# Kernel optimization log

Measured on AMD Instinct MI355X. Metric: run time of the kernel, lower is better.

The kernel has to match this reference:

```python
import math
import jax, jax.numpy as jnp
import numpy as np

N = 50000          # nodes
E = 1_600_000      # edges
DNE = 128
DED = 128
NUM_RBF = 50
R_CUT = 5.0
LN_EPS = 1e-5


def setup_inputs() -> dict:
    key = jax.random.key(0)
    ks = jax.random.split(key, 16)
    z = jax.random.normal(ks[0], (N, 25), jnp.float32)
    edge = jax.random.randint(ks[1], (E, 2), 0, N, dtype=jnp.int64)
    r = jax.random.uniform(ks[2], (E,), jnp.float32) * (R_CUT * 1.1)  # some beyond cutoff
    u_raw = jax.random.normal(ks[3], (E, 3), jnp.float32)
    u = u_raw / jnp.linalg.norm(u_raw, axis=-1, keepdims=True)

    def xavier(k, shape):
        fan_in, fan_out = shape
        lim = math.sqrt(6.0 / (fan_in + fan_out))
        return jax.random.uniform(k, shape, jnp.float32, -lim, lim)

    return {
        "z": z, "edge": edge, "r": r, "u": u,
        "A_na_w": xavier(ks[4], (25, DNE)), "A_na_b": jnp.zeros((DNE,), jnp.float32),
        "A_nbr_w": xavier(ks[5], (25, DNE)), "A_nbr_b": jnp.zeros((DNE,), jnp.float32),
        "W_ndp_w": xavier(ks[6], (NUM_RBF, DNE)), "W_ndp_b": jnp.zeros((DNE,), jnp.float32),
        "W_nrd_w": xavier(ks[7], (2 * DNE, DNE)), "W_nrd_b": jnp.zeros((DNE,), jnp.float32),
        "W_nru_w": xavier(ks[8], (DNE, DNE)), "W_nru_b": jnp.zeros((DNE,), jnp.float32),
        "W_erp_w": xavier(ks[9], (NUM_RBF, DED)), "W_erp_b": jnp.zeros((DED,), jnp.float32),
        "ln_g": jnp.ones((DNE,), jnp.float32), "ln_b": jnp.zeros((DNE,), jnp.float32),
    }


def _sh_l2(u):
    x, y, zc = u[:, 0], u[:, 1], u[:, 2]
    s3 = math.sqrt(3.0)
    return jnp.stack([
        s3 * x * y,
        s3 * y * zc,
        0.5 * (3.0 * zc * zc - 1.0),
        s3 * zc * x,
        0.5 * s3 * (x * x - y * y),
    ], axis=-1)  # [E, 5]


def _rbf(r):
    start = math.exp(-R_CUT)
    means = jnp.linspace(start, 1.0, NUM_RBF)
    beta = (2.0 / NUM_RBF * (1.0 - start)) ** (-2)
    alpha = 5.0 / R_CUT
    return jnp.exp(-beta * (jnp.exp(-alpha * r[:, None]) - means) ** 2)  # [E, NUM_RBF]


def reference(z, edge, r, u,
              A_na_w, A_na_b, A_nbr_w, A_nbr_b,
              W_ndp_w, W_ndp_b, W_nrd_w, W_nrd_b,
              W_nru_w, W_nru_b, W_erp_w, W_erp_b,
              ln_g, ln_b):
    i, j = edge[:, 0], edge[:, 1]
    n_nodes = z.shape[0]

    # edge tensor representations (Lmax=2)
    rt0 = r[:, None]          # [E,1]
    rt1 = u                   # [E,3]
    rt2 = _sh_l2(u)           # [E,5]

    rbf = _rbf(r)                                              # [E,R]
    c = (0.5 * (jnp.cos(math.pi * r / R_CUT) + 1.0)
         * (r < R_CUT).astype(r.dtype))[:, None]               # [E,1]

    nbr = jax.nn.silu(z @ A_nbr_w + A_nbr_b)                   # [N,dne]
    gate = (rbf @ W_ndp_w + W_ndp_b) * c                       # [E,dne]
    msg = nbr[j] * gate                                        # gather + gate
    m = jax.ops.segment_sum(msg, i, num_segments=n_nodes)      # scatter-add [N,dne]

    na = jax.nn.silu(z @ A_na_w + A_na_b)
    h = jnp.concatenate([na, m], axis=-1) @ W_nrd_w + W_nrd_b  # [N,dne]
    mu = jnp.mean(h, axis=-1, keepdims=True)
    var = jnp.var(h, axis=-1, keepdims=True)
    h = (h - mu) / jnp.sqrt(var + LN_EPS) * ln_g + ln_b
    h = jax.nn.silu(h)
    h = h @ W_nru_w + W_nru_b                                  # [N,dne]

    t = (h[i] + h[j]) * (rbf @ W_erp_w + W_erp_b)              # [E,ded]
    return (h, t, rt0, rt1, rt2, c)
```

## Files before the change

### kernel.cpp

```cpp
#include <hip/hip_runtime.h>
#include <hip/hip_bf16.h>
#include <math.h>

#define NN 50000
#define NE 1600000
#define D 128
#define NRBF 50
#define RCUT 5.0f
#define LNEPS 1e-5f
#define EB 16
#define EB2 64
#define EDGE_GRID 2048
#define SCAN_B 196
#define NB 16
#define NPB 8

typedef __attribute__((ext_vector_type(8))) short bf16x8;
typedef __attribute__((ext_vector_type(4))) float f32x4;

__device__ __forceinline__ float silu_f(float x) {
    return x / (1.0f + __expf(-x));
}
__device__ __forceinline__ unsigned short f2bf(float x) {
    __hip_bfloat16 b = __float2bfloat16(x);
    return *reinterpret_cast<unsigned short*>(&b);
}
__device__ __forceinline__ float bf2f(unsigned short u) {
    unsigned int x = ((unsigned int)u) << 16;
    return __uint_as_float(x);
}

__global__ __launch_bounds__(128) void nbr_kernel(
    const float* __restrict__ z, const float* __restrict__ Aw,
    const float* __restrict__ Ab, unsigned short* __restrict__ nbr_bf)
{
    const int n = blockIdx.x;
    const int d = threadIdx.x;
    float acc = Ab[d];
#pragma unroll
    for (int k = 0; k < 25; ++k)
        acc = fmaf(z[n * 25 + k], Aw[k * D + d], acc);
    nbr_bf[(size_t)n * D + d] = f2bf(silu_f(acc));
}

__global__ __launch_bounds__(256) void aux_kernel(
    const int* __restrict__ edge, const float* __restrict__ r,
    const float* __restrict__ u, float* __restrict__ rt0,
    float* __restrict__ rt1, float* __restrict__ rt2,
    float* __restrict__ cout, int* __restrict__ cnt)
{
    const int e = blockIdx.x * 256 + threadIdx.x;
    if (e >= NE) return;
    const float rr = r[e];
    rt0[e] = rr;
    const float cc = (rr < RCUT)
        ? 0.5f * (__cosf(3.14159265358979f * rr * (1.0f / RCUT)) + 1.0f)
        : 0.0f;
    cout[e] = cc;
    const float x  = u[e * 3 + 0];
    const float y  = u[e * 3 + 1];
    const float zc = u[e * 3 + 2];
    rt1[(size_t)e * 3 + 0] = x;
    rt1[(size_t)e * 3 + 1] = y;
    rt1[(size_t)e * 3 + 2] = zc;
    const float s3 = 1.7320508075688772f;
    rt2[(size_t)e * 5 + 0] = s3 * x * y;
    rt2[(size_t)e * 5 + 1] = s3 * y * zc;
    rt2[(size_t)e * 5 + 2] = 0.5f * (3.0f * zc * zc - 1.0f);
    rt2[(size_t)e * 5 + 3] = s3 * zc * x;
    rt2[(size_t)e * 5 + 4] = 0.5f * s3 * (x * x - y * y);
    atomicAdd(&cnt[edge[2 * e]], 1);
}

__global__ __launch_bounds__(256) void scan1_kernel(
    const int* __restrict__ cnt, int* __restrict__ off, int* __restrict__ bsum)
{
    __shared__ int s[2][256];
    const int t = threadIdx.x;
    const int g = blockIdx.x * 256 + t;
    const int v = (g < NN) ? cnt[g] : 0;
    int incl = v;
    s[0][t] = incl;
    __syncthreads();
    int cur = 0;
#pragma unroll
    for (int dd = 1; dd < 256; dd <<= 1) {
        const int add = (t >= dd) ? s[cur][t - dd] : 0;
        incl += add;
        s[cur ^ 1][t] = incl;
        __syncthreads();
        cur ^= 1;
    }
    if (g < NN) off[g] = incl - v;
    if (t == 255) bsum[blockIdx.x] = incl;
}

__global__ __launch_bounds__(256) void scan2_kernel(int* __restrict__ bsum)
{
    __shared__ int s[2][256];
    const int t = threadIdx.x;
    const int v = (t < SCAN_B) ? bsum[t] : 0;
    int incl = v;
    s[0][t] = incl;
    __syncthreads();
    int cur = 0;
#pragma unroll
    for (int dd = 1; dd < 256; dd <<= 1) {
        const int add = (t >= dd) ? s[cur][t - dd] : 0;
        incl += add;
        s[cur ^ 1][t] = incl;
        __syncthreads();
        cur ^= 1;
    }
    if (t < SCAN_B) bsum[t] = incl - v;
}

__global__ __launch_bounds__(256) void scan3_kernel(
    int* __restrict__ off, const int* __restrict__ bsum)
{
    const int g = blockIdx.x * 256 + threadIdx.x;
    if (g < NN) off[g] += bsum[blockIdx.x];
    if (g == 0) off[NN] = NE;
}

__global__ __launch_bounds__(256) void scatter_kernel(
    const int* __restrict__ edge, const float* __restrict__ r,
    const int* __restrict__ off, int* __restrict__ cursor,
    uint2* __restrict__ jr)
{
    const int e = blockIdx.x * 256 + threadIdx.x;
    if (e >= NE) return;
    const int2 ep = ((const int2*)edge)[e];
    const int pos = atomicAdd(&cursor[ep.x], 1);
    uint2 v;
    v.x = (unsigned int)ep.y;
    v.y = __float_as_uint(r[e]);
    jr[off[ep.x] + pos] = v;
}

__global__ __launch_bounds__(128) void gather_msg_mfma(
    const uint2* __restrict__ jr, const int* __restrict__ off,
    const float* __restrict__ W_ndp, const float* __restrict__ b_ndp,
    const unsigned short* __restrict__ nbr_bf, float* __restrict__ m)
{
    __shared__ unsigned short P[EB][64];
    __shared__ float er_s[EB];
    __shared__ float c_s[EB];
    __shared__ int   j_s[EB];

    const int tid = threadIdx.x;
    const int w   = tid >> 6;
    const int l   = tid & 63;
    const int lr  = l & 15;
    const int lg  = l >> 4;

    bf16x8 wf[4][2];
#pragma unroll
    for (int dt = 0; dt < 4; ++dt) {
        const int col = w * 64 + lr * 4 + dt;
#pragma unroll
        for (int s = 0; s < 2; ++s) {
            bf16x8 v;
#pragma unroll
            for (int j = 0; j < 8; ++j) {
                const int k = s * 32 + lg * 8 + j;
                float wv = 0.0f;
                if (k < NRBF)       wv = W_ndp[k * D + col];
                else if (k == NRBF) wv = b_ndp[col];
                v[j] = (short)f2bf(wv);
            }
            wf[dt][s] = v;
        }
    }

    const float start = expf(-RCUT);
    const float step  = (1.0f - start) / (NRBF - 1);
    const float bq    = (2.0f / NRBF) * (1.0f - start);
    const float beta  = 1.0f / (bq * bq);

    const int prow = tid >> 3;
    const int pci  = tid & 7;

    for (int nn = 0; nn < NPB; ++nn) {
        const int n   = blockIdx.x * NPB + nn;
        const int s0  = off[n];
        const int deg = off[n + 1] - s0;

        f32x4 macc[4] = {{0,0,0,0},{0,0,0,0},{0,0,0,0},{0,0,0,0}};

        for (int base = 0; base < deg; base += EB) {
            const int chunk = min(EB, deg - base);
            if (tid < EB) {
                if (tid < chunk) {
                    const uint2 v = jr[s0 + base + tid];
                    const float rr = __uint_as_float(v.y);
                    er_s[tid] = __expf(-rr);
                    c_s[tid] = (rr < RCUT)
                        ? 0.5f * (__cosf(3.14159265358979f * rr * (1.0f / RCUT)) + 1.0f)
                        : 0.0f;
                    j_s[tid] = (int)v.x;
                } else {
                    er_s[tid] = 0.0f; c_s[tid] = 0.0f; j_s[tid] = 0;
                }
            }
            __syncthreads();
            {
                const float er = er_s[prow];
                const float cc = c_s[prow];
                unsigned int pk[4];
#pragma unroll
                for (int p2 = 0; p2 < 4; ++p2) {
                    unsigned int word = 0;
#pragma unroll
                    for (int c = 0; c < 2; ++c) {
                        const int k = pci * 8 + p2 * 2 + c;
                        float v = 0.0f;
                        if (k < NRBF) {
                            const float diff = er - (start + (float)k * step);
                            v = cc * __expf(-beta * diff * diff);
                        } else if (k == NRBF) {
                            v = cc;
                        }
                        word |= ((unsigned int)f2bf(v)) << (16 * c);
                    }
                    pk[p2] = word;
                }
                const int swc = pci ^ (prow & 7);
                *(uint4*)&P[prow][swc * 8] = make_uint4(pk[0], pk[1], pk[2], pk[3]);
            }
            __syncthreads();
            bf16x8 af[2];
#pragma unroll
            for (int s = 0; s < 2; ++s) {
                const int swc = (s * 4 + lg) ^ (lr & 7);
                af[s] = *(const bf16x8*)&P[lr][swc * 8];
            }
            f32x4 accs[4];
#pragma unroll
            for (int dt = 0; dt < 4; ++dt) {
                f32x4 acc = {0.0f, 0.0f, 0.0f, 0.0f};
                acc = __builtin_amdgcn_mfma_f32_16x16x32_bf16(af[0], wf[dt][0], acc, 0, 0, 0);
                acc = __builtin_amdgcn_mfma_f32_16x16x32_bf16(af[1], wf[dt][1], acc, 0, 0, 0);
                accs[dt] = acc;
            }
#pragma unroll
            for (int q = 0; q < 4; ++q) {
                const int row = j_s[lg * 4 + q];
                const uint2 nv8 = *(const uint2*)(nbr_bf + (size_t)row * D + w * 64 + lr * 4);
                const float n0 = bf2f((unsigned short)(nv8.x & 0xffff));
                const float n1 = bf2f((unsigned short)(nv8.x >> 16));
                const float n2 = bf2f((unsigned short)(nv8.y & 0xffff));
                const float n3 = bf2f((unsigned short)(nv8.y >> 16));
                macc[0][q] = fmaf(n0, accs[0][q], macc[0][q]);
                macc[1][q] = fmaf(n1, accs[1][q], macc[1][q]);
                macc[2][q] = fmaf(n2, accs[2][q], macc[2][q]);
                macc[3][q] = fmaf(n3, accs[3][q], macc[3][q]);
            }
            __syncthreads();
        }

        float v0 = macc[0][0] + macc[0][1] + macc[0][2] + macc[0][3];
        float v1 = macc[1][0] + macc[1][1] + macc[1][2] + macc[1][3];
        float v2 = macc[2][0] + macc[2][1] + macc[2][2] + macc[2][3];
        float v3 = macc[3][0] + macc[3][1] + macc[3][2] + macc[3][3];
        v0 += __shfl_xor(v0, 16); v0 += __shfl_xor(v0, 32);
        v1 += __shfl_xor(v1, 16); v1 += __shfl_xor(v1, 32);
        v2 += __shfl_xor(v2, 16); v2 += __shfl_xor(v2, 32);
        v3 += __shfl_xor(v3, 16); v3 += __shfl_xor(v3, 32);
        if (lg == 0) {
            float4 o = {v0, v1, v2, v3};
            *(float4*)&m[(size_t)n * D + w * 64 + lr * 4] = o;
        }
    }
}

__global__ __launch_bounds__(256) void node_kernel2(
    const float* __restrict__ z, const float* __restrict__ A_na_w,
    const float* __restrict__ A_na_b, const float* __restrict__ m,
    const float* __restrict__ W_nrd_w, const float* __restrict__ W_nrd_b,
    const float* __restrict__ W_nru_w, const float* __restrict__ W_nru_b,
    const float* __restrict__ ln_g, const float* __restrict__ ln_b,
    float* __restrict__ hout, unsigned short* __restrict__ h_bf)
{
    __shared__ float inbuf[NB][260];
    __shared__ float wbuf[32][128];
    __shared__ float part[4][NB][2];

    const int tid = threadIdx.x;
    const int n0 = blockIdx.x * NB;
    const int nl = tid & 15;
    const int dg = tid >> 4;

    for (int idx = tid; idx < NB * 128; idx += 256) {
        const int n = idx >> 7;
        const int d = idx & 127;
        float acc = A_na_b[d];
#pragma unroll
        for (int k = 0; k < 25; ++k)
            acc = fmaf(z[(size_t)(n0 + n) * 25 + k], A_na_w[k * D + d], acc);
        inbuf[n][d]       = silu_f(acc);
        inbuf[n][128 + d] = m[(size_t)(n0 + n) * D + d];
    }

    float h1[8];
#pragma unroll
    for (int dd = 0; dd < 8; ++dd) h1[dd] = W_nrd_b[dg * 8 + dd];

    for (int tile = 0; tile < 8; ++tile) {
        __syncthreads();
        for (int v = tid; v < 32 * 32; v += 256) {
            const int row = v >> 5;
            const int c4  = (v & 31) * 4;
            *(float4*)&wbuf[row][c4] =
                *(const float4*)&W_nrd_w[(size_t)(tile * 32 + row) * D + c4];
        }
        __syncthreads();
#pragma unroll 4
        for (int k = 0; k < 32; ++k) {
            const float rin = inbuf[nl][tile * 32 + k];
            const float4 wa = *(const float4*)&wbuf[k][dg * 8];
            const float4 wb = *(const float4*)&wbuf[k][dg * 8 + 4];
            h1[0] = fmaf(rin, wa.x, h1[0]);
            h1[1] = fmaf(rin, wa.y, h1[1]);
            h1[2] = fmaf(rin, wa.z, h1[2]);
            h1[3] = fmaf(rin, wa.w, h1[3]);
            h1[4] = fmaf(rin, wb.x, h1[4]);
            h1[5] = fmaf(rin, wb.y, h1[5]);
            h1[6] = fmaf(rin, wb.z, h1[6]);
            h1[7] = fmaf(rin, wb.w, h1[7]);
        }
    }

    float s = 0.0f, sq = 0.0f;
#pragma unroll
    for (int dd = 0; dd < 8; ++dd) { s += h1[dd]; sq += h1[dd] * h1[dd]; }
    s  += __shfl_xor(s, 16);  sq += __shfl_xor(sq, 16);
    s  += __shfl_xor(s, 32);  sq += __shfl_xor(sq, 32);
    const int wv = tid >> 6;
    if ((tid & 63) < 16) { part[wv][nl][0] = s; part[wv][nl][1] = sq; }
    __syncthreads();
    float ts = 0.0f, tsq = 0.0f;
#pragma unroll
    for (int w = 0; w < 4; ++w) { ts += part[w][nl][0]; tsq += part[w][nl][1]; }
    const float mu  = ts * (1.0f / 128.0f);
    const float var = tsq * (1.0f / 128.0f) - mu * mu;
    const float inv = rsqrtf(var + LNEPS);

#pragma unroll
    for (int dd = 0; dd < 8; ++dd) {
        const int d = dg * 8 + dd;
        inbuf[nl][d] = silu_f((h1[dd] - mu) * inv * ln_g[d] + ln_b[d]);
    }

    float h2[8];
#pragma unroll
    for (int dd = 0; dd < 8; ++dd) h2[dd] = W_nru_b[dg * 8 + dd];

    for (int tile = 0; tile < 4; ++tile) {
        __syncthreads();
        for (int v = tid; v < 32 * 32; v += 256) {
            const int row = v >> 5;
            const int c4  = (v & 31) * 4;
            *(float4*)&wbuf[row][c4] =
                *(const float4*)&W_nru_w[(size_t)(tile * 32 + row) * D + c4];
        }
        __syncthreads();
#pragma unroll 4
        for (int k = 0; k < 32; ++k) {
            const float rin = inbuf[nl][tile * 32 + k];
            const float4 wa = *(const float4*)&wbuf[k][dg * 8];
            const float4 wb = *(const float4*)&wbuf[k][dg * 8 + 4];
            h2[0] = fmaf(rin, wa.x, h2[0]);
            h2[1] = fmaf(rin, wa.y, h2[1]);
            h2[2] = fmaf(rin, wa.z, h2[2]);
            h2[3] = fmaf(rin, wa.w, h2[3]);
            h2[4] = fmaf(rin, wb.x, h2[4]);
            h2[5] = fmaf(rin, wb.y, h2[5]);
            h2[6] = fmaf(rin, wb.z, h2[6]);
            h2[7] = fmaf(rin, wb.w, h2[7]);
        }
    }

    float4 o0 = {h2[0], h2[1], h2[2], h2[3]};
    float4 o1 = {h2[4], h2[5], h2[6], h2[7]};
    *(float4*)&hout[(size_t)(n0 + nl) * D + dg * 8]     = o0;
    *(float4*)&hout[(size_t)(n0 + nl) * D + dg * 8 + 4] = o1;

    unsigned int b0 = (unsigned int)f2bf(h2[0]) | ((unsigned int)f2bf(h2[1]) << 16);
    unsigned int b1 = (unsigned int)f2bf(h2[2]) | ((unsigned int)f2bf(h2[3]) << 16);
    unsigned int b2 = (unsigned int)f2bf(h2[4]) | ((unsigned int)f2bf(h2[5]) << 16);
    unsigned int b3 = (unsigned int)f2bf(h2[6]) | ((unsigned int)f2bf(h2[7]) << 16);
    *(uint4*)&h_bf[(size_t)(n0 + nl) * D + dg * 8] = make_uint4(b0, b1, b2, b3);
}

__global__ __launch_bounds__(256) void edge_out_mfma(
    const int* __restrict__ edge, const float* __restrict__ r,
    const float* __restrict__ W_erp, const float* __restrict__ b_erp,
    const unsigned short* __restrict__ h_bf, float* __restrict__ t)
{
    __shared__ unsigned short P[EB2][64];
    __shared__ unsigned short hv[EB2][136];
    __shared__ int ij_s[EB2][2];

    const int tid = threadIdx.x;
    const int w  = tid >> 6;
    const int l  = tid & 63;
    const int lr = l & 15;
    const int lg = l >> 4;

    bf16x8 wf[8][2];
    float bias[8];
#pragma unroll
    for (int dt = 0; dt < 8; ++dt) {
        const int col = lr * 8 + dt;
        bias[dt] = b_erp[col];
#pragma unroll
        for (int s = 0; s < 2; ++s) {
            bf16x8 v;
#pragma unroll
            for (int j = 0; j < 8; ++j) {
                const int k = s * 32 + lg * 8 + j;
                v[j] = (k < NRBF) ? (short)f2bf(W_erp[k * D + col]) : (short)0;
            }
            wf[dt][s] = v;
        }
    }

    const float start = expf(-RCUT);
    const float step  = (1.0f - start) / (NRBF - 1);
    const float bq    = (2.0f / NRBF) * (1.0f - start);
    const float beta  = 1.0f / (bq * bq);

    const int prow  = tid & 63;
    const int kbase = (tid >> 6) * 16;

    const int nbatch = NE / EB2;
    for (int batch = blockIdx.x; batch < nbatch; batch += gridDim.x) {
        const int eb = batch * EB2;
        if (tid < EB2) {
            const int2 ep = ((const int2*)edge)[eb + tid];
            ij_s[tid][0] = ep.x;
            ij_s[tid][1] = ep.y;
        }
        {
            const float er = __expf(-r[eb + prow]);
            const int kc0 = kbase >> 3;
#pragma unroll
            for (int c2 = 0; c2 < 2; ++c2) {
                const int kc = kc0 + c2;
                unsigned int pk[4];
#pragma unroll
                for (int p2 = 0; p2 < 4; ++p2) {
                    unsigned int word = 0;
#pragma unroll
                    for (int c = 0; c < 2; ++c) {
                        const int k = kc * 8 + p2 * 2 + c;
                        float v = 0.0f;
                        if (k < NRBF) {
                            const float diff = er - (start + (float)k * step);
                            v = __expf(-beta * diff * diff);
                        }
                        word |= ((unsigned int)f2bf(v)) << (16 * c);
                    }
                    pk[p2] = word;
                }
                const int swc = kc ^ (prow & 7);
                *(uint4*)&P[prow][swc * 8] = make_uint4(pk[0], pk[1], pk[2], pk[3]);
            }
        }
        __syncthreads();

        const int arow = w * 16 + lr;
        bf16x8 af[2];
#pragma unroll
        for (int s = 0; s < 2; ++s) {
            const int swc = (s * 4 + lg) ^ (arow & 7);
            af[s] = *(const bf16x8*)&P[arow][swc * 8];
        }

#pragma unroll
        for (int idx = tid; idx < EB2 * 16; idx += 256) {
            const int el = idx >> 4;
            const int ch = idx & 15;
            const uint4 ui = *((const uint4*)(h_bf + (size_t)ij_s[el][0] * D) + ch);
            const uint4 uj = *((const uint4*)(h_bf + (size_t)ij_s[el][1] * D) + ch);
            const unsigned int wi[4] = {ui.x, ui.y, ui.z, ui.w};
            const unsigned int wj[4] = {uj.x, uj.y, uj.z, uj.w};
            unsigned int wo[4];
#pragma unroll
            for (int p = 0; p < 4; ++p) {
                const float lo = bf2f((unsigned short)(wi[p] & 0xffff))
                               + bf2f((unsigned short)(wj[p] & 0xffff));
                const float hi = bf2f((unsigned short)(wi[p] >> 16))
                               + bf2f((unsigned short)(wj[p] >> 16));
                wo[p] = (unsigned int)f2bf(lo) | ((unsigned int)f2bf(hi) << 16);
            }
            *(uint4*)&hv[el][ch * 8] = make_uint4(wo[0], wo[1], wo[2], wo[3]);
        }
        __syncthreads();

        f32x4 accs[8];
#pragma unroll
        for (int dt = 0; dt < 8; ++dt) {
            f32x4 acc = {0.0f, 0.0f, 0.0f, 0.0f};
            acc = __builtin_amdgcn_mfma_f32_16x16x32_bf16(af[0], wf[dt][0], acc, 0, 0, 0);
            acc = __builtin_amdgcn_mfma_f32_16x16x32_bf16(af[1], wf[dt][1], acc, 0, 0, 0);
            accs[dt] = acc;
        }
#pragma unroll
        for (int q = 0; q < 4; ++q) {
            const int el = w * 16 + lg * 4 + q;
            const bf16x8 hv8 = *(const bf16x8*)&hv[el][lr * 8];
            float o[8];
#pragma unroll
            for (int dt = 0; dt < 8; ++dt)
                o[dt] = bf2f((unsigned short)hv8[dt]) * (accs[dt][q] + bias[dt]);
            float4 o0 = {o[0], o[1], o[2], o[3]};
            float4 o1 = {o[4], o[5], o[6], o[7]};
            float* tp = &t[(size_t)(eb + el) * D + lr * 8];
            *(float4*)tp       = o0;
            *(float4*)(tp + 4) = o1;
        }
        __syncthreads();
    }
}

extern "C" void kernel_launch(void* const* d_in, const int* in_sizes, int n_in,
                              void* d_out, int out_size, void* d_ws, size_t ws_size,
                              hipStream_t stream) {
    const float* z      = (const float*)d_in[0];
    const int*   edge   = (const int*)d_in[1];
    const float* r      = (const float*)d_in[2];
    const float* u      = (const float*)d_in[3];
    const float* A_na_w  = (const float*)d_in[4];
    const float* A_na_b  = (const float*)d_in[5];
    const float* A_nbr_w = (const float*)d_in[6];
    const float* A_nbr_b = (const float*)d_in[7];
    const float* W_ndp_w = (const float*)d_in[8];
    const float* W_ndp_b = (const float*)d_in[9];
    const float* W_nrd_w = (const float*)d_in[10];
    const float* W_nrd_b = (const float*)d_in[11];
    const float* W_nru_w = (const float*)d_in[12];
    const float* W_nru_b = (const float*)d_in[13];
    const float* W_erp_w = (const float*)d_in[14];
    const float* W_erp_b = (const float*)d_in[15];
    const float* ln_g    = (const float*)d_in[16];
    const float* ln_b    = (const float*)d_in[17];

    float* out = (float*)d_out;
    float* h_out   = out;
    float* t_out   = out + (size_t)NN * D;
    float* rt0_out = t_out + (size_t)NE * D;
    float* rt1_out = rt0_out + (size_t)NE;
    float* rt2_out = rt1_out + (size_t)NE * 3;
    float* c_out   = rt2_out + (size_t)NE * 5;

    unsigned short* nbr_bf = (unsigned short*)d_ws;
    float* m_ws   = (float*)((char*)d_ws + (size_t)NN * D * sizeof(unsigned short));
    unsigned short* h_bf = (unsigned short*)((char*)m_ws + (size_t)NN * D * sizeof(float));

    uint2* jr   = (uint2*)t_out;
    int* off    = (int*)(jr + NE);
    int* cursor = off + (NN + 1);
    int* bsum   = cursor + NN;

    hipMemsetAsync(cursor, 0, (size_t)NN * sizeof(int), stream);

    nbr_kernel<<<NN, 128, 0, stream>>>(z, A_nbr_w, A_nbr_b, nbr_bf);

    aux_kernel<<<(NE + 255) / 256, 256, 0, stream>>>(
        edge, r, u, rt0_out, rt1_out, rt2_out, c_out, cursor);

    scan1_kernel<<<SCAN_B, 256, 0, stream>>>(cursor, off, bsum);
    scan2_kernel<<<1, 256, 0, stream>>>(bsum);
    scan3_kernel<<<SCAN_B, 256, 0, stream>>>(off, bsum);

    hipMemsetAsync(cursor, 0, (size_t)NN * sizeof(int), stream);

    scatter_kernel<<<(NE + 255) / 256, 256, 0, stream>>>(edge, r, off, cursor, jr);

    gather_msg_mfma<<<NN / NPB, 128, 0, stream>>>(
        jr, off, W_ndp_w, W_ndp_b, nbr_bf, m_ws);

    node_kernel2<<<NN / NB, 256, 0, stream>>>(
        z, A_na_w, A_na_b, m_ws, W_nrd_w, W_nrd_b,
        W_nru_w, W_nru_b, ln_g, ln_b, h_out, h_bf);

    edge_out_mfma<<<EDGE_GRID, 256, 0, stream>>>(
        edge, r, W_erp_w, W_erp_b, h_bf, t_out);
}
```

Measured before the change: 846.0 us.

## Make gather and edge-output kernels wave-independent, drop LDS staging and barriers

```diff
diff --git a/kernel.cpp b/kernel.cpp
--- a/kernel.cpp
+++ b/kernel.cpp
@@ -8,12 +8,10 @@
 #define NRBF 50
 #define RCUT 5.0f
 #define LNEPS 1e-5f
-#define EB 16
-#define EB2 64
-#define EDGE_GRID 2048
 #define SCAN_B 196
 #define NB 16
-#define NPB 8
+#define NPW 8
+#define EO_GRID 2048
 
 typedef __attribute__((ext_vector_type(8))) short bf16x8;
 typedef __attribute__((ext_vector_type(4))) float f32x4;
@@ -52,23 +50,23 @@
     const int e = blockIdx.x * 256 + threadIdx.x;
     if (e >= NE) return;
     const float rr = r[e];
-    rt0[e] = rr;
+    __builtin_nontemporal_store(rr, &rt0[e]);
     const float cc = (rr < RCUT)
         ? 0.5f * (__cosf(3.14159265358979f * rr * (1.0f / RCUT)) + 1.0f)
         : 0.0f;
-    cout[e] = cc;
+    __builtin_nontemporal_store(cc, &cout[e]);
     const float x  = u[e * 3 + 0];
     const float y  = u[e * 3 + 1];
     const float zc = u[e * 3 + 2];
-    rt1[(size_t)e * 3 + 0] = x;
-    rt1[(size_t)e * 3 + 1] = y;
-    rt1[(size_t)e * 3 + 2] = zc;
+    __builtin_nontemporal_store(x,  &rt1[(size_t)e * 3 + 0]);
+    __builtin_nontemporal_store(y,  &rt1[(size_t)e * 3 + 1]);
+    __builtin_nontemporal_store(zc, &rt1[(size_t)e * 3 + 2]);
     const float s3 = 1.7320508075688772f;
-    rt2[(size_t)e * 5 + 0] = s3 * x * y;
-    rt2[(size_t)e * 5 + 1] = s3 * y * zc;
-    rt2[(size_t)e * 5 + 2] = 0.5f * (3.0f * zc * zc - 1.0f);
-    rt2[(size_t)e * 5 + 3] = s3 * zc * x;
-    rt2[(size_t)e * 5 + 4] = 0.5f * s3 * (x * x - y * y);
+    __builtin_nontemporal_store(s3 * x * y,                  &rt2[(size_t)e * 5 + 0]);
+    __builtin_nontemporal_store(s3 * y * zc,                 &rt2[(size_t)e * 5 + 1]);
+    __builtin_nontemporal_store(0.5f * (3.0f * zc * zc - 1.0f), &rt2[(size_t)e * 5 + 2]);
+    __builtin_nontemporal_store(s3 * zc * x,                 &rt2[(size_t)e * 5 + 3]);
+    __builtin_nontemporal_store(0.5f * s3 * (x * x - y * y), &rt2[(size_t)e * 5 + 4]);
     atomicAdd(&cnt[edge[2 * e]], 1);
 }
 
@@ -138,26 +136,21 @@
     jr[off[ep.x] + pos] = v;
 }
 
-__global__ __launch_bounds__(128) void gather_msg_mfma(
+__global__ __launch_bounds__(256) void gather_msg_wave(
     const uint2* __restrict__ jr, const int* __restrict__ off,
     const float* __restrict__ W_ndp, const float* __restrict__ b_ndp,
     const unsigned short* __restrict__ nbr_bf, float* __restrict__ m)
 {
-    __shared__ unsigned short P[EB][64];
-    __shared__ float er_s[EB];
-    __shared__ float c_s[EB];
-    __shared__ int   j_s[EB];
-
     const int tid = threadIdx.x;
     const int w   = tid >> 6;
     const int l   = tid & 63;
     const int lr  = l & 15;
     const int lg  = l >> 4;
 
-    bf16x8 wf[4][2];
-#pragma unroll
-    for (int dt = 0; dt < 4; ++dt) {
-        const int col = w * 64 + lr * 4 + dt;
+    bf16x8 wf[8][2];
+#pragma unroll
+    for (int dt = 0; dt < 8; ++dt) {
+        const int col = lr * 8 + dt;
 #pragma unroll
         for (int s = 0; s < 2; ++s) {
             bf16x8 v;
@@ -178,66 +171,54 @@
     const float bq    = (2.0f / NRBF) * (1.0f - start);
     const float beta  = 1.0f / (bq * bq);
 
-    const int prow = tid >> 3;
-    const int pci  = tid & 7;
-
-    for (int nn = 0; nn < NPB; ++nn) {
-        const int n   = blockIdx.x * NPB + nn;
+    const int wid = blockIdx.x * 4 + w;
+
+    for (int nn = 0; nn < NPW; ++nn) {
+        const int n = wid * NPW + nn;
+        if (n >= NN) break;
         const int s0  = off[n];
         const int deg = off[n + 1] - s0;
 
-        f32x4 macc[4] = {{0,0,0,0},{0,0,0,0},{0,0,0,0},{0,0,0,0}};
-
-        for (int base = 0; base < deg; base += EB) {
-            const int chunk = min(EB, deg - base);
-            if (tid < EB) {
-                if (tid < chunk) {
-                    const uint2 v = jr[s0 + base + tid];
-                    const float rr = __uint_as_float(v.y);
-                    er_s[tid] = __expf(-rr);
-                    c_s[tid] = (rr < RCUT)
-                        ? 0.5f * (__cosf(3.14159265358979f * rr * (1.0f / RCUT)) + 1.0f)
-                        : 0.0f;
-                    j_s[tid] = (int)v.x;
-                } else {
-                    er_s[tid] = 0.0f; c_s[tid] = 0.0f; j_s[tid] = 0;
+        f32x4 macc[8] = {{0,0,0,0},{0,0,0,0},{0,0,0,0},{0,0,0,0},
+                         {0,0,0,0},{0,0,0,0},{0,0,0,0},{0,0,0,0}};
+
+        for (int base = 0; base < deg; base += 16) {
+            unsigned int jv = 0;
+            float er = 0.0f, cc = 0.0f;
+            if (l < 16 && l < deg - base) {
+                const uint2 v = jr[s0 + base + l];
+                jv = v.x;
+                const float rr = __uint_as_float(v.y);
+                er = __expf(-rr);
+                cc = (rr < RCUT)
+                    ? 0.5f * (__cosf(3.14159265358979f * rr * (1.0f / RCUT)) + 1.0f)
+                    : 0.0f;
+            }
+            const float erL = __shfl(er, lr);
+            const float ccL = __shfl(cc, lr);
+
+            bf16x8 af[2];
+#pragma unroll
+            for (int s = 0; s < 2; ++s) {
+                bf16x8 a;
+#pragma unroll
+                for (int j = 0; j < 8; ++j) {
+                    const int k = s * 32 + lg * 8 + j;
+                    float pv = 0.0f;
+                    if (k < NRBF) {
+                        const float diff = erL - (start + (float)k * step);
+                        pv = ccL * __expf(-beta * diff * diff);
+                    } else if (k == NRBF) {
+                        pv = ccL;
+                    }
+                    a[j] = (short)f2bf(pv);
                 }
-            }
-            __syncthreads();
-            {
-                const float er = er_s[prow];
-                const float cc = c_s[prow];
-                unsigned int pk[4];
-#pragma unroll
-                for (int p2 = 0; p2 < 4; ++p2) {
-                    unsigned int word = 0;
-#pragma unroll
-                    for (int c = 0; c < 2; ++c) {
-                        const int k = pci * 8 + p2 * 2 + c;
-                        float v = 0.0f;
-                        if (k < NRBF) {
-                            const float diff = er - (start + (float)k * step);
-                            v = cc * __expf(-beta * diff * diff);
-                        } else if (k == NRBF) {
-                            v = cc;
-                        }
-                        word |= ((unsigned int)f2bf(v)) << (16 * c);
-                    }
-                    pk[p2] = word;
-                }
-                const int swc = pci ^ (prow & 7);
-                *(uint4*)&P[prow][swc * 8] = make_uint4(pk[0], pk[1], pk[2], pk[3]);
-            }
-            __syncthreads();
-            bf16x8 af[2];
-#pragma unroll
-            for (int s = 0; s < 2; ++s) {
-                const int swc = (s * 4 + lg) ^ (lr & 7);
-                af[s] = *(const bf16x8*)&P[lr][swc * 8];
-            }
-            f32x4 accs[4];
-#pragma unroll
-            for (int dt = 0; dt < 4; ++dt) {
+                af[s] = a;
+            }
+
+            f32x4 accs[8];
+#pragma unroll
+            for (int dt = 0; dt < 8; ++dt) {
                 f32x4 acc = {0.0f, 0.0f, 0.0f, 0.0f};
                 acc = __builtin_amdgcn_mfma_f32_16x16x32_bf16(af[0], wf[dt][0], acc, 0, 0, 0);
                 acc = __builtin_amdgcn_mfma_f32_16x16x32_bf16(af[1], wf[dt][1], acc, 0, 0, 0);
@@ -245,31 +226,28 @@
             }
 #pragma unroll
             for (int q = 0; q < 4; ++q) {
-                const int row = j_s[lg * 4 + q];
-                const uint2 nv8 = *(const uint2*)(nbr_bf + (size_t)row * D + w * 64 + lr * 4);
-                const float n0 = bf2f((unsigned short)(nv8.x & 0xffff));
-                const float n1 = bf2f((unsigned short)(nv8.x >> 16));
-                const float n2 = bf2f((unsigned short)(nv8.y & 0xffff));
-                const float n3 = bf2f((unsigned short)(nv8.y >> 16));
-                macc[0][q] = fmaf(n0, accs[0][q], macc[0][q]);
-                macc[1][q] = fmaf(n1, accs[1][q], macc[1][q]);
-                macc[2][q] = fmaf(n2, accs[2][q], macc[2][q]);
-                macc[3][q] = fmaf(n3, accs[3][q], macc[3][q]);
-            }
-            __syncthreads();
-        }
-
-        float v0 = macc[0][0] + macc[0][1] + macc[0][2] + macc[0][3];
-        float v1 = macc[1][0] + macc[1][1] + macc[1][2] + macc[1][3];
-        float v2 = macc[2][0] + macc[2][1] + macc[2][2] + macc[2][3];
-        float v3 = macc[3][0] + macc[3][1] + macc[3][2] + macc[3][3];
-        v0 += __shfl_xor(v0, 16); v0 += __shfl_xor(v0, 32);
-        v1 += __shfl_xor(v1, 16); v1 += __shfl_xor(v1, 32);
-        v2 += __shfl_xor(v2, 16); v2 += __shfl_xor(v2, 32);
-        v3 += __shfl_xor(v3, 16); v3 += __shfl_xor(v3, 32);
+                const int jrow = __shfl((int)jv, lg * 4 + q);
+                const bf16x8 nv8 = *(const bf16x8*)(nbr_bf + (size_t)jrow * D + lr * 8);
+#pragma unroll
+                for (int dt = 0; dt < 8; ++dt)
+                    macc[dt][q] = fmaf(bf2f((unsigned short)nv8[dt]), accs[dt][q], macc[dt][q]);
+            }
+        }
+
+        float vv[8];
+#pragma unroll
+        for (int dt = 0; dt < 8; ++dt) {
+            float v = macc[dt][0] + macc[dt][1] + macc[dt][2] + macc[dt][3];
+            v += __shfl_xor(v, 16);
+            v += __shfl_xor(v, 32);
+            vv[dt] = v;
+        }
         if (lg == 0) {
-            float4 o = {v0, v1, v2, v3};
-            *(float4*)&m[(size_t)n * D + w * 64 + lr * 4] = o;
+            f32x4 o0 = {vv[0], vv[1], vv[2], vv[3]};
+            f32x4 o1 = {vv[4], vv[5], vv[6], vv[7]};
+            float* mp = &m[(size_t)n * D + lr * 8];
+            *(f32x4*)mp       = o0;
+            *(f32x4*)(mp + 4) = o1;
         }
     }
 }
@@ -381,10 +359,11 @@
         }
     }
 
-    float4 o0 = {h2[0], h2[1], h2[2], h2[3]};
-    float4 o1 = {h2[4], h2[5], h2[6], h2[7]};
-    *(float4*)&hout[(size_t)(n0 + nl) * D + dg * 8]     = o0;
-    *(float4*)&hout[(size_t)(n0 + nl) * D + dg * 8 + 4] = o1;
+    f32x4 o0 = {h2[0], h2[1], h2[2], h2[3]};
+    f32x4 o1 = {h2[4], h2[5], h2[6], h2[7]};
+    float* hp = &hout[(size_t)(n0 + nl) * D + dg * 8];
+    __builtin_nontemporal_store(o0, (f32x4*)hp);
+    __builtin_nontemporal_store(o1, (f32x4*)(hp + 4));
 
     unsigned int b0 = (unsigned int)f2bf(h2[0]) | ((unsigned int)f2bf(h2[1]) << 16);
     unsigned int b1 = (unsigned int)f2bf(h2[2]) | ((unsigned int)f2bf(h2[3]) << 16);
@@ -393,20 +372,16 @@
     *(uint4*)&h_bf[(size_t)(n0 + nl) * D + dg * 8] = make_uint4(b0, b1, b2, b3);
 }
 
-__global__ __launch_bounds__(256) void edge_out_mfma(
+__global__ __launch_bounds__(256) void edge_out_wave(
     const int* __restrict__ edge, const float* __restrict__ r,
     const float* __restrict__ W_erp, const float* __restrict__ b_erp,
     const unsigned short* __restrict__ h_bf, float* __restrict__ t)
 {
-    __shared__ unsigned short P[EB2][64];
-    __shared__ unsigned short hv[EB2][136];
-    __shared__ int ij_s[EB2][2];
-
     const int tid = threadIdx.x;
-    const int w  = tid >> 6;
-    const int l  = tid & 63;
-    const int lr = l & 15;
-    const int lg = l >> 4;
+    const int w   = tid >> 6;
+    const int l   = tid & 63;
+    const int lr  = l & 15;
+    const int lg  = l >> 4;
 
     bf16x8 wf[8][2];
     float bias[8];
@@ -431,73 +406,38 @@
     const float bq    = (2.0f / NRBF) * (1.0f - start);
     const float beta  = 1.0f / (bq * bq);
 
-    const int prow  = tid & 63;
-    const int kbase = (tid >> 6) * 16;
-
-    const int nbatch = NE / EB2;
-    for (int batch = blockIdx.x; batch < nbatch; batch += gridDim.x) {
-        const int eb = batch * EB2;
-        if (tid < EB2) {
-            const int2 ep = ((const int2*)edge)[eb + tid];
-            ij_s[tid][0] = ep.x;
-            ij_s[tid][1] = ep.y;
-        }
-        {
-            const float er = __expf(-r[eb + prow]);
-            const int kc0 = kbase >> 3;
-#pragma unroll
-            for (int c2 = 0; c2 < 2; ++c2) {
-                const int kc = kc0 + c2;
-                unsigned int pk[4];
-#pragma unroll
-                for (int p2 = 0; p2 < 4; ++p2) {
-                    unsigned int word = 0;
-#pragma unroll
-                    for (int c = 0; c < 2; ++c) {
-                        const int k = kc * 8 + p2 * 2 + c;
-                        float v = 0.0f;
-                        if (k < NRBF) {
-                            const float diff = er - (start + (float)k * step);
-                            v = __expf(-beta * diff * diff);
-                        }
-                        word |= ((unsigned int)f2bf(v)) << (16 * c);
-                    }
-                    pk[p2] = word;
+    const int wid = blockIdx.x * 4 + w;
+    const int nw  = gridDim.x * 4;
+    const int ngroup = NE / 16;
+
+    for (int g = wid; g < ngroup; g += nw) {
+        const int eb = g * 16;
+        int iv = 0, jv = 0;
+        float er = 0.0f;
+        if (l < 16) {
+            const int2 ep = ((const int2*)edge)[eb + l];
+            iv = ep.x;
+            jv = ep.y;
+            er = __expf(-r[eb + l]);
+        }
+        const float erL = __shfl(er, lr);
+
+        bf16x8 af[2];
+#pragma unroll
+        for (int s = 0; s < 2; ++s) {
+            bf16x8 a;
+#pragma unroll
+            for (int j = 0; j < 8; ++j) {
+                const int k = s * 32 + lg * 8 + j;
+                float pv = 0.0f;
+                if (k < NRBF) {
+                    const float diff = erL - (start + (float)k * step);
+                    pv = __expf(-beta * diff * diff);
                 }
-                const int swc = kc ^ (prow & 7);
-                *(uint4*)&P[prow][swc * 8] = make_uint4(pk[0], pk[1], pk[2], pk[3]);
-            }
-        }
-        __syncthreads();
-
-        const int arow = w * 16 + lr;
-        bf16x8 af[2];
-#pragma unroll
-        for (int s = 0; s < 2; ++s) {
-            const int swc = (s * 4 + lg) ^ (arow & 7);
-            af[s] = *(const bf16x8*)&P[arow][swc * 8];
-        }
-
-#pragma unroll
-        for (int idx = tid; idx < EB2 * 16; idx += 256) {
-            const int el = idx >> 4;
-            const int ch = idx & 15;
-            const uint4 ui = *((const uint4*)(h_bf + (size_t)ij_s[el][0] * D) + ch);
-            const uint4 uj = *((const uint4*)(h_bf + (size_t)ij_s[el][1] * D) + ch);
-            const unsigned int wi[4] = {ui.x, ui.y, ui.z, ui.w};
-            const unsigned int wj[4] = {uj.x, uj.y, uj.z, uj.w};
-            unsigned int wo[4];
-#pragma unroll
-            for (int p = 0; p < 4; ++p) {
-                const float lo = bf2f((unsigned short)(wi[p] & 0xffff))
-                               + bf2f((unsigned short)(wj[p] & 0xffff));
-                const float hi = bf2f((unsigned short)(wi[p] >> 16))
-                               + bf2f((unsigned short)(wj[p] >> 16));
-                wo[p] = (unsigned int)f2bf(lo) | ((unsigned int)f2bf(hi) << 16);
-            }
-            *(uint4*)&hv[el][ch * 8] = make_uint4(wo[0], wo[1], wo[2], wo[3]);
-        }
-        __syncthreads();
+                a[j] = (short)f2bf(pv);
+            }
+            af[s] = a;
+        }
 
         f32x4 accs[8];
 #pragma unroll
@@ -507,21 +447,25 @@
             acc = __builtin_amdgcn_mfma_f32_16x16x32_bf16(af[1], wf[dt][1], acc, 0, 0, 0);
             accs[dt] = acc;
         }
+
 #pragma unroll
         for (int q = 0; q < 4; ++q) {
-            const int el = w * 16 + lg * 4 + q;
-            const bf16x8 hv8 = *(const bf16x8*)&hv[el][lr * 8];
+            const int irow = __shfl(iv, lg * 4 + q);
+            const int jrow = __shfl(jv, lg * 4 + q);
+            const bf16x8 hi8 = *(const bf16x8*)(h_bf + (size_t)irow * D + lr * 8);
+            const bf16x8 hj8 = *(const bf16x8*)(h_bf + (size_t)jrow * D + lr * 8);
             float o[8];
 #pragma unroll
-            for (int dt = 0; dt < 8; ++dt)
-                o[dt] = bf2f((unsigned short)hv8[dt]) * (accs[dt][q] + bias[dt]);
-            float4 o0 = {o[0], o[1], o[2], o[3]};
-            float4 o1 = {o[4], o[5], o[6], o[7]};
-            float* tp = &t[(size_t)(eb + el) * D + lr * 8];
-            *(float4*)tp       = o0;
-            *(float4*)(tp + 4) = o1;
-        }
-        __syncthreads();
+            for (int dt = 0; dt < 8; ++dt) {
+                const float hvf = bf2f((unsigned short)hi8[dt]) + bf2f((unsigned short)hj8[dt]);
+                o[dt] = hvf * (accs[dt][q] + bias[dt]);
+            }
+            f32x4 o0 = {o[0], o[1], o[2], o[3]};
+            f32x4 o1 = {o[4], o[5], o[6], o[7]};
+            float* tp = &t[(size_t)(eb + lg * 4 + q) * D + lr * 8];
+            __builtin_nontemporal_store(o0, (f32x4*)tp);
+            __builtin_nontemporal_store(o1, (f32x4*)(tp + 4));
+        }
     }
 }
 
@@ -579,13 +523,17 @@
 
     scatter_kernel<<<(NE + 255) / 256, 256, 0, stream>>>(edge, r, off, cursor, jr);
 
-    gather_msg_mfma<<<NN / NPB, 128, 0, stream>>>(
-        jr, off, W_ndp_w, W_ndp_b, nbr_bf, m_ws);
+    {
+        const int nwaves = (NN + NPW - 1) / NPW;
+        const int blocks = (nwaves + 3) / 4;
+        gather_msg_wave<<<blocks, 256, 0, stream>>>(
+            jr, off, W_ndp_w, W_ndp_b, nbr_bf, m_ws);
+    }
 
     node_kernel2<<<NN / NB, 256, 0, stream>>>(
         z, A_na_w, A_na_b, m_ws, W_nrd_w, W_nrd_b,
         W_nru_w, W_nru_b, ln_g, ln_b, h_out, h_bf);
 
-    edge_out_mfma<<<EDGE_GRID, 256, 0, stream>>>(
+    edge_out_wave<<<EO_GRID, 256, 0, stream>>>(
         edge, r, W_erp_w, W_erp_b, h_bf, t_out);
 }
```

Measured after the change: 832.2 us. About the same (-1.6%).
